# Kernel tuning notes

Measured on AMD Instinct MI355X. Metric: run time of the kernel, lower is better.

The kernel has to match this reference:

```python
import math
import jax, jax.numpy as jnp
import numpy as np

B, L, NS = 8, 1024, 512
D, NH, DN = 512, 8, 256
E, K, HE = 8, 2, 2048
EPS = 1e-5


def setup_inputs() -> dict:
    key = jax.random.key(0)
    ks = jax.random.split(key, 40)
    def rn(i, shape, s=0.02):
        return jax.random.normal(ks[i], shape, jnp.float32) * s
    inp = {
        'x': jax.random.normal(ks[0], (B, L, D), jnp.float32),
        'scene_tokens': jax.random.normal(ks[1], (B, NS, D), jnp.float32),
        't': jax.random.uniform(ks[2], (B,), jnp.float32) * 1000.0,
        # scene LayerNorm (affine)
        'scene_norm_g': jnp.ones((D,), jnp.float32),
        'scene_norm_b': jnp.zeros((D,), jnp.float32),
        # scene cross-attn projections (stored [in,out])
        'ca_wq': rn(3, (D, D)), 'ca_bq': jnp.zeros((D,)),
        'ca_wk': rn(4, (D, D)), 'ca_bk': jnp.zeros((D,)),
        'ca_wv': rn(5, (D, D)), 'ca_bv': jnp.zeros((D,)),
        'ca_wo': rn(6, (D, D)), 'ca_bo': jnp.zeros((D,)),
        # self-attn projections
        'sa_wq': rn(7, (D, D)), 'sa_bq': jnp.zeros((D,)),
        'sa_wk': rn(8, (D, D)), 'sa_bk': jnp.zeros((D,)),
        'sa_wv': rn(9, (D, D)), 'sa_bv': jnp.zeros((D,)),
        'sa_wo': rn(10, (D, D)), 'sa_bo': jnp.zeros((D,)),
        # noise_embed MLP: Linear(D,DN) -> SiLU -> Linear(DN,DN)
        'ne_w1': rn(11, (D, DN)), 'ne_b1': jnp.zeros((DN,)),
        'ne_w2': rn(12, (DN, DN)), 'ne_b2': jnp.zeros((DN,)),
        # AdaLN modulations: Linear(DN, 2D)
        'ncsa_mod_w': rn(13, (DN, 2 * D)), 'ncsa_mod_b': jnp.zeros((2 * D,)),
        'moe_mod_w': rn(14, (DN, 2 * D)), 'moe_mod_b': jnp.zeros((2 * D,)),
        # router
        'router_w': rn(15, (DN, E), s=0.1),
        # stacked pose-branch experts: fc_in D->2*HE, fc_out HE->D
        'fc_in_w': rn(16, (E, D, 2 * HE)), 'fc_in_b': jnp.zeros((E, 2 * HE)),
        'fc_out_w': rn(17, (E, HE, D)), 'fc_out_b': jnp.zeros((E, D)),
    }
    return inp


def _ln(x):
    mu = x.mean(-1, keepdims=True)
    var = ((x - mu) ** 2).mean(-1, keepdims=True)
    return (x - mu) * jax.lax.rsqrt(var + EPS)


def _mha(q_in, k_in, v_in, wq, bq, wk, bk, wv, bv, wo, bo):
    b, lq, d = q_in.shape
    lk = k_in.shape[1]
    hd = d // NH
    q = (q_in @ wq + bq).reshape(b, lq, NH, hd)
    k = (k_in @ wk + bk).reshape(b, lk, NH, hd)
    v = (v_in @ wv + bv).reshape(b, lk, NH, hd)
    att = jnp.einsum('bqhd,bkhd->bhqk', q, k) / math.sqrt(hd)
    p = jax.nn.softmax(att, axis=-1)
    o = jnp.einsum('bhqk,bkhd->bqhd', p, v).reshape(b, lq, d)
    return o @ wo + bo


def reference(x, scene_tokens, t,
              scene_norm_g, scene_norm_b,
              ca_wq, ca_bq, ca_wk, ca_bk, ca_wv, ca_bv, ca_wo, ca_bo,
              sa_wq, sa_bq, sa_wk, sa_bk, sa_wv, sa_bv, sa_wo, sa_bo,
              ne_w1, ne_b1, ne_w2, ne_b2,
              ncsa_mod_w, ncsa_mod_b, moe_mod_w, moe_mod_b,
              router_w, fc_in_w, fc_in_b, fc_out_w, fc_out_b):
    # --- noise clock embedding: sinusoidal(t, D) -> MLP ---
    half = D // 2
    freqs = jnp.exp(-math.log(10000.0) * jnp.arange(half, dtype=jnp.float32) / (half - 1))
    ang = t[:, None] * freqs[None, :]
    temb = jnp.concatenate([jnp.cos(ang), jnp.sin(ang)], axis=-1)  # [B, D]
    nc = jax.nn.silu(temb @ ne_w1 + ne_b1) @ ne_w2 + ne_b2  # [B, DN]

    # --- scene cross-attention ---
    x_in = _ln(x) * scene_norm_g + scene_norm_b
    x = x + _mha(x_in, scene_tokens, scene_tokens,
                 ca_wq, ca_bq, ca_wk, ca_bk, ca_wv, ca_bv, ca_wo, ca_bo)

    # --- noise-conditioned self-attention (AdaLN) ---
    mod = nc @ ncsa_mod_w + ncsa_mod_b
    shift, scale = jnp.split(mod, 2, axis=-1)
    x_ncsa = _ln(x) * (1.0 + scale[:, None, :]) + shift[:, None, :]
    x = x + _mha(x_ncsa, x_ncsa, x_ncsa,
                 sa_wq, sa_bq, sa_wk, sa_bk, sa_wv, sa_bv, sa_wo, sa_bo)

    # --- pose branch: AdaLN + noise-conditioned MoE ---
    mod = nc @ moe_mod_w + moe_mod_b
    shift, scale = jnp.split(mod, 2, axis=-1)
    x_moe = _ln(x) * (1.0 + scale[:, None, :]) + shift[:, None, :]

    logits = nc @ router_w  # temperature = 1.0
    probs = jax.nn.softmax(logits, axis=-1)
    tw, ti = jax.lax.top_k(probs, K)  # [B,K]
    tw = tw / jnp.clip(tw.sum(-1, keepdims=True), 1e-8)

    # gather per-sample selected expert weights -> grouped GEMM
    Wi = fc_in_w[ti]   # [B,K,D,2HE]
    bi = fc_in_b[ti]   # [B,K,2HE]
    h = jnp.einsum('bld,bkdh->bklh', x_moe, Wi) + bi[:, :, None, :]
    val, gate = jnp.split(h, 2, axis=-1)
    hid = val * jax.nn.silu(gate)   # [B,K,L,HE]
    Wo = fc_out_w[ti]  # [B,K,HE,D]
    bo = fc_out_b[ti]  # [B,K,D]
    eo = jnp.einsum('bklh,bkhd->bkld', hid, Wo) + bo[:, :, None, :]
    mixed = jnp.einsum('bk,bkld->bld', tw, eo)

    return x + mixed
```

## Files before the change

kernel.cpp:

```cpp
#include <hip/hip_runtime.h>
#include <math.h>

typedef unsigned short ushort_t;
typedef __attribute__((ext_vector_type(8))) short short8;
typedef __attribute__((ext_vector_type(4))) float f32x4;

#define B_   8
#define L_   1024
#define NS_  512
#define D_   512
#define NH_  8
#define HE_  2048
#define EPS_ 1e-5f

#define MFMA16(a, b, c) __builtin_amdgcn_mfma_f32_16x16x32_bf16(a, b, c, 0, 0, 0)
#define GL2LDS(g, l) __builtin_amdgcn_global_load_lds( \
    (const __attribute__((address_space(1))) unsigned int*)(g), \
    (__attribute__((address_space(3))) unsigned int*)(l), 16, 0, 0)

__device__ __forceinline__ ushort_t f2bf(float f) {
  unsigned u = __float_as_uint(f);
  unsigned r = (u + 0x7fffu + ((u >> 16) & 1u)) >> 16;
  return (ushort_t)r;
}

__device__ __forceinline__ void stage_tile(const ushort_t* __restrict__ g0,
                                           int ld, ushort_t* lds) {
  const int t = threadIdx.x;
  const int w = t >> 6, lane = t & 63;
#pragma unroll
  for (int j = 0; j < 2; ++j) {
    const int c = w * 64 + j * 256 + lane;
    const int row = c >> 2, col = (c & 3) * 8;
    GL2LDS(g0 + (size_t)row * ld + col, lds + (size_t)(w * 64 + j * 256) * 8);
  }
}

__device__ __forceinline__ void stage_tile64(const ushort_t* __restrict__ g0,
                                             int ld, ushort_t* lds) {
  const int t = threadIdx.x;
  const int w = t >> 6, lane = t & 63;
#pragma unroll
  for (int j = 0; j < 4; ++j) {
    const int c = w * 64 + j * 256 + lane;
    const int row = c >> 3;
    const int sc = (c & 7) ^ (row & 7);
    GL2LDS(g0 + (size_t)row * ld + sc * 8, lds + (size_t)(w * 64 + j * 256) * 8);
  }
}

__global__ __launch_bounds__(1024) void noise_embed(
    const float* __restrict__ t_in,
    const float* __restrict__ w1, const float* __restrict__ b1,
    const float* __restrict__ w2, const float* __restrict__ b2,
    const float* __restrict__ rw,
    float* __restrict__ nc_out,
    float* __restrict__ tw_out, int* __restrict__ ti_out)
{
  const int b = blockIdx.x;
  const int t = threadIdx.x;
  __shared__ float temb[512];
  __shared__ float h1[256];
  __shared__ float ncs[256];
  __shared__ float lg[8];
  const float tv = t_in[b];
  if (t < 512) {
    const int k = t & 255;
    float fr = __expf(-logf(10000.0f) * (float)k / 255.0f);
    float ang = tv * fr;
    temb[t] = (t < 256) ? cosf(ang) : sinf(ang);
  }
  __syncthreads();
  const int col = t >> 2, part = t & 3;
  {
    float s = 0.f;
    const float* wp = w1 + (size_t)(part * 128) * 256 + col;
    const float* tp = temb + part * 128;
#pragma unroll 32
    for (int i = 0; i < 128; ++i) s += tp[i] * wp[(size_t)i * 256];
    s += __shfl_xor(s, 1, 64);
    s += __shfl_xor(s, 2, 64);
    if (part == 0) {
      s += b1[col];
      h1[col] = s / (1.0f + __expf(-s));
    }
  }
  __syncthreads();
  {
    float s = 0.f;
    const float* wp = w2 + (size_t)(part * 64) * 256 + col;
    const float* hp = h1 + part * 64;
#pragma unroll 32
    for (int i = 0; i < 64; ++i) s += hp[i] * wp[(size_t)i * 256];
    s += __shfl_xor(s, 1, 64);
    s += __shfl_xor(s, 2, 64);
    if (part == 0) {
      s += b2[col];
      ncs[col] = s;
      nc_out[b * 256 + col] = s;
    }
  }
  __syncthreads();
  if (t < 64) {
    const int e = t >> 3, seg = t & 7;
    float s = 0.f;
#pragma unroll
    for (int i = 0; i < 32; ++i) s += ncs[seg * 32 + i] * rw[(seg * 32 + i) * 8 + e];
    s += __shfl_xor(s, 1, 64);
    s += __shfl_xor(s, 2, 64);
    s += __shfl_xor(s, 4, 64);
    if (seg == 0) lg[e] = s;
  }
  __syncthreads();
  if (t == 0) {
    float mx = lg[0];
    for (int e = 1; e < 8; ++e) mx = fmaxf(mx, lg[e]);
    float z = 0.f, p[8];
    for (int e = 0; e < 8; ++e) { p[e] = __expf(lg[e] - mx); z += p[e]; }
    for (int e = 0; e < 8; ++e) p[e] /= z;
    int i0 = 0;
    for (int e = 1; e < 8; ++e) if (p[e] > p[i0]) i0 = e;
    int i1 = (i0 == 0) ? 1 : 0;
    for (int e = 0; e < 8; ++e) if (e != i0 && p[e] > p[i1]) i1 = e;
    float s01 = fmaxf(p[i0] + p[i1], 1e-8f);
    tw_out[b * 2 + 0] = p[i0] / s01;
    tw_out[b * 2 + 1] = p[i1] / s01;
    ti_out[b * 2 + 0] = i0;
    ti_out[b * 2 + 1] = i1;
  }
}

__global__ __launch_bounds__(1024) void mod_proj(
    const float* __restrict__ nc,
    const float* __restrict__ ncsa_w, const float* __restrict__ ncsa_b,
    const float* __restrict__ moe_w, const float* __restrict__ moe_b,
    float* __restrict__ ncsa_mod, float* __restrict__ moe_mod)
{
  const int b = blockIdx.x, cg = blockIdx.y;
  const int t = threadIdx.x;
  __shared__ float ncs[256];
  if (t < 256) ncs[t] = nc[b * 256 + t];
  __syncthreads();
  const int idx = t >> 2, part = t & 3;
  const int half = idx >> 7;
  const int col = cg * 128 + (idx & 127);
  const float* wsel = half ? moe_w : ncsa_w;
  float s = 0.f;
  const float* wp = wsel + (size_t)(part * 64) * 1024 + col;
  const float* np = ncs + part * 64;
#pragma unroll 32
  for (int i = 0; i < 64; ++i) s += np[i] * wp[(size_t)i * 1024];
  s += __shfl_xor(s, 1, 64);
  s += __shfl_xor(s, 2, 64);
  if (part == 0) {
    const float* bsel = half ? moe_b : ncsa_b;
    float* osel = half ? moe_mod : ncsa_mod;
    osel[b * 1024 + col] = s + bsel[col];
  }
}

__global__ __launch_bounds__(256) void ln_mod_kernel(
    const float* __restrict__ X, const float* __restrict__ gvec,
    const float* __restrict__ bvec, const float* __restrict__ mod,
    ushort_t* __restrict__ Y)
{
  const int row = blockIdx.x;
  const int b = row >> 10;
  const int t = threadIdx.x;
  const float* xr = X + (size_t)row * 512;
  float2 v = *(const float2*)(xr + t * 2);
  float s = v.x + v.y;
  float q = v.x * v.x + v.y * v.y;
#pragma unroll
  for (int off = 32; off > 0; off >>= 1) {
    s += __shfl_down(s, off, 64);
    q += __shfl_down(q, off, 64);
  }
  __shared__ float ws_[4], wq_[4], smu[1], sinv[1];
  if ((t & 63) == 0) { ws_[t >> 6] = s; wq_[t >> 6] = q; }
  __syncthreads();
  if (t == 0) {
    float S = ws_[0] + ws_[1] + ws_[2] + ws_[3];
    float Q = wq_[0] + wq_[1] + wq_[2] + wq_[3];
    float mu = S * (1.0f / 512.0f);
    float var = Q * (1.0f / 512.0f) - mu * mu;
    smu[0] = mu;
    sinv[0] = rsqrtf(var + EPS_);
  }
  __syncthreads();
  const float mu = smu[0], inv = sinv[0];
  const int d0 = t * 2;
  float scx, scy, shx, shy;
  if (mod) {
    const float* mrow = mod + (size_t)b * 1024;
    scx = 1.0f + mrow[512 + d0]; scy = 1.0f + mrow[512 + d0 + 1];
    shx = mrow[d0];              shy = mrow[d0 + 1];
  } else {
    scx = gvec[d0]; scy = gvec[d0 + 1];
    shx = bvec[d0]; shy = bvec[d0 + 1];
  }
  float ox = (v.x - mu) * inv * scx + shx;
  float oy = (v.y - mu) * inv * scy + shy;
  unsigned pk = (unsigned)f2bf(ox) | ((unsigned)f2bf(oy) << 16);
  *(unsigned*)(Y + (size_t)row * 512 + d0) = pk;
}

__global__ __launch_bounds__(256) void transpose_cvt(
    const float* __restrict__ in, ushort_t* __restrict__ out,
    int R, int C, long ibs, long obs)
{
  __shared__ float tile[32][33];
  const float* src = in + (size_t)blockIdx.z * ibs;
  ushort_t* dst = out + (size_t)blockIdx.z * obs;
  const int c0 = blockIdx.x * 32, r0 = blockIdx.y * 32;
  const int tx = threadIdx.x & 31, ty = threadIdx.x >> 5;
  for (int rr = ty; rr < 32; rr += 8)
    tile[rr][tx] = src[(size_t)(r0 + rr) * C + c0 + tx];
  __syncthreads();
  for (int rr = ty; rr < 32; rr += 8)
    dst[(size_t)(c0 + rr) * R + r0 + tx] = f2bf(tile[tx][rr]);
}

struct P8 { const float* p[8]; };
__global__ __launch_bounds__(256) void transpose_cvt8(
    P8 srcs, ushort_t* __restrict__ out)
{
  __shared__ float tile[32][33];
  const float* src = srcs.p[blockIdx.z];
  ushort_t* dst = out + (size_t)blockIdx.z * 512 * 512;
  const int c0 = blockIdx.x * 32, r0 = blockIdx.y * 32;
  const int tx = threadIdx.x & 31, ty = threadIdx.x >> 5;
  for (int rr = ty; rr < 32; rr += 8)
    tile[rr][tx] = src[(size_t)(r0 + rr) * 512 + c0 + tx];
  __syncthreads();
  for (int rr = ty; rr < 32; rr += 8)
    dst[(size_t)(c0 + rr) * 512 + r0 + tx] = f2bf(tile[tx][rr]);
}

__global__ __launch_bounds__(256) void cvt_bf16(
    const float* __restrict__ in, ushort_t* __restrict__ out)
{
  const int i = (blockIdx.x * 256 + threadIdx.x) * 4;
  float4 v = *(const float4*)(in + i);
  uint2 pk;
  pk.x = (unsigned)f2bf(v.x) | ((unsigned)f2bf(v.y) << 16);
  pk.y = (unsigned)f2bf(v.z) | ((unsigned)f2bf(v.w) << 16);
  *(uint2*)(out + i) = pk;
}

struct B3 { const float* p[3]; };
__global__ __launch_bounds__(256) void gemm_bf16(
    const ushort_t* __restrict__ A, const ushort_t* __restrict__ Bt,
    B3 bias, const float* __restrict__ resid,
    void* __restrict__ Cout, int M, int N, int K, int bf16_out)
{
  __shared__ ushort_t As[2][8192];
  __shared__ ushort_t Bs[2][8192];
  const int t = threadIdx.x;
  const int w = t >> 6, lane = t & 63;
  const int quad = lane >> 4, r = lane & 15;
  const int sw = r & 7;
  const int wm = w >> 1, wn = w & 1;
  const int gx = gridDim.x;
  const int T = gx * gridDim.y;
  const int lid = blockIdx.x + gx * blockIdx.y;
  const int nl = (lid & 7) * (T >> 3) + (lid >> 3);
  const int bm = (nl / gx) * 128, bn = (nl % gx) * 128;
  f32x4 acc[4][4];
#pragma unroll
  for (int i = 0; i < 4; ++i)
#pragma unroll
    for (int j = 0; j < 4; ++j) acc[i][j] = (f32x4){0.f, 0.f, 0.f, 0.f};
  const ushort_t* Ab = A + (size_t)bm * K;
  const ushort_t* Bb = Bt + (size_t)bn * K;
  const int NIT = K >> 6;
  stage_tile64(Ab, K, As[0]);
  stage_tile64(Bb, K, Bs[0]);
  __syncthreads();
  for (int it = 0; it < NIT; ++it) {
    const int cur = it & 1;
    if (it + 1 < NIT) {
      stage_tile64(Ab + (it + 1) * 64, K, As[cur ^ 1]);
      stage_tile64(Bb + (it + 1) * 64, K, Bs[cur ^ 1]);
    }
#pragma unroll
    for (int ki = 0; ki < 2; ++ki) {
      const int ch = (((ki << 2) | quad) ^ sw) * 8;
      short8 af[4], bfg[4];
#pragma unroll
      for (int i = 0; i < 4; ++i)
        af[i] = *(const short8*)&As[cur][(wm * 64 + i * 16 + r) * 64 + ch];
#pragma unroll
      for (int j = 0; j < 4; ++j)
        bfg[j] = *(const short8*)&Bs[cur][(wn * 64 + j * 16 + r) * 64 + ch];
#pragma unroll
      for (int i = 0; i < 4; ++i)
#pragma unroll
        for (int j = 0; j < 4; ++j)
          acc[i][j] = MFMA16(af[i], bfg[j], acc[i][j]);
    }
    __syncthreads();
  }
  if (bf16_out) {
    ushort_t* Cb = (ushort_t*)Cout;
#pragma unroll
    for (int j = 0; j < 4; ++j) {
      const int col = bn + wn * 64 + j * 16 + r;
      const float bia = bias.p[col >> 9][col & 511];
#pragma unroll
      for (int i = 0; i < 4; ++i)
#pragma unroll
        for (int reg = 0; reg < 4; ++reg) {
          const int row = bm + wm * 64 + i * 16 + quad * 4 + reg;
          Cb[(size_t)row * N + col] = f2bf(acc[i][j][reg] + bia);
        }
    }
  } else {
    float* Cf = (float*)Cout;
#pragma unroll
    for (int j = 0; j < 4; ++j) {
      const int col = bn + wn * 64 + j * 16 + r;
      const float bia = bias.p[col >> 9][col & 511];
#pragma unroll
      for (int i = 0; i < 4; ++i)
#pragma unroll
        for (int reg = 0; reg < 4; ++reg) {
          const int row = bm + wm * 64 + i * 16 + quad * 4 + reg;
          float v = acc[i][j][reg] + bia;
          if (resid) v += resid[(size_t)row * N + col];
          Cf[(size_t)row * N + col] = v;
        }
    }
  }
}

__global__ __launch_bounds__(512, 4) void fattn_mfma(
    const ushort_t* __restrict__ Q, const ushort_t* __restrict__ Kmat,
    const ushort_t* __restrict__ V, ushort_t* __restrict__ O, int Lk,
    int ldq, int ldkv)
{
  __shared__ __align__(16) ushort_t Ks[64][72];
  __shared__ __align__(16) ushort_t Vt[64][72];
  __shared__ __align__(16) ushort_t Pt[8][16][72];
  const int t = threadIdx.x;
  const int w = t >> 6, lane = t & 63;
  const int quad = lane >> 4, r = lane & 15;
  const int bid = blockIdx.x;
  const int xcd = bid & 7, jj = bid >> 3;
  const int qi = jj & 7;
  const int g = xcd + 8 * (jj >> 3);
  const int h = g & 7, b = g >> 3;
  const int q0 = qi * 128;
  const size_t hoff = (size_t)h * 64;
  const ushort_t* Qb = Q + ((size_t)b * 1024 + q0) * ldq + hoff;
  const ushort_t* Kb = Kmat + (size_t)b * Lk * ldkv + hoff;
  const ushort_t* Vb = V + (size_t)b * Lk * ldkv + hoff;

  short8 qb[2];
#pragma unroll
  for (int ki = 0; ki < 2; ++ki)
    qb[ki] = *(const short8*)(Qb + (size_t)(w * 16 + r) * ldq +
                              ki * 32 + quad * 8);

  f32x4 oacc[4];
#pragma unroll
  for (int rt = 0; rt < 4; ++rt) oacc[rt] = (f32x4){0.f, 0.f, 0.f, 0.f};
  float m_ = -1e30f;
  float l_ = 0.f;

  uint4 kr, vr, kn, vn;
  const int dof = w * 8;
  auto ldkvf = [&](int k0, uint4& kp, uint4& vp) {
    kp = *(const uint4*)(Kb + (size_t)(k0 + lane) * ldkv + dof);
    vp = *(const uint4*)(Vb + (size_t)(k0 + lane) * ldkv + dof);
  };
  auto stkv = [&](const uint4& kp, const uint4& vp) {
    *(uint4*)&Ks[lane][dof] = kp;
    const ushort_t* vv = (const ushort_t*)&vp;
#pragma unroll
    for (int i = 0; i < 8; ++i) Vt[dof + i][lane] = vv[i];
  };

  ldkvf(0, kr, vr);
  const int nch = Lk >> 6;
  for (int c = 0; c < nch; ++c) {
    stkv(kr, vr);
    __syncthreads();
    if (c + 1 < nch) ldkvf((c + 1) << 6, kn, vn);

    f32x4 sacc[4];
#pragma unroll
    for (int rt = 0; rt < 4; ++rt) sacc[rt] = (f32x4){0.f, 0.f, 0.f, 0.f};
    __builtin_amdgcn_s_setprio(1);
#pragma unroll
    for (int ki = 0; ki < 2; ++ki) {
      short8 kf[4];
#pragma unroll
      for (int rt = 0; rt < 4; ++rt)
        kf[rt] = *(const short8*)&Ks[rt * 16 + r][ki * 32 + quad * 8];
#pragma unroll
      for (int rt = 0; rt < 4; ++rt)
        sacc[rt] = MFMA16(kf[rt], qb[ki], sacc[rt]);
    }
    __builtin_amdgcn_s_setprio(0);

    {
      float vmax = sacc[0][0];
#pragma unroll
      for (int rt = 0; rt < 4; ++rt)
#pragma unroll
        for (int reg = 0; reg < 4; ++reg) vmax = fmaxf(vmax, sacc[rt][reg]);
      vmax = fmaxf(vmax, __shfl_xor(vmax, 16, 64));
      vmax = fmaxf(vmax, __shfl_xor(vmax, 32, 64));
      const float pm = vmax * 0.125f;
      if (__any(pm > m_ + 8.f)) {
        const float mnew = fmaxf(m_, pm);
        const float corr = __expf(m_ - mnew);
        m_ = mnew;
        l_ *= corr;
#pragma unroll
        for (int rt = 0; rt < 4; ++rt)
#pragma unroll
          for (int reg = 0; reg < 4; ++reg) oacc[rt][reg] *= corr;
      }
      const float mcur = m_;
      float ps = 0.f;
#pragma unroll
      for (int rt = 0; rt < 4; ++rt) {
        float p0 = __expf(fmaf(sacc[rt][0], 0.125f, -mcur));
        float p1 = __expf(fmaf(sacc[rt][1], 0.125f, -mcur));
        float p2 = __expf(fmaf(sacc[rt][2], 0.125f, -mcur));
        float p3 = __expf(fmaf(sacc[rt][3], 0.125f, -mcur));
        ps += (p0 + p1) + (p2 + p3);
        uint2 pk;
        pk.x = (unsigned)f2bf(p0) | ((unsigned)f2bf(p1) << 16);
        pk.y = (unsigned)f2bf(p2) | ((unsigned)f2bf(p3) << 16);
        *(uint2*)&Pt[w][r][rt * 16 + quad * 4] = pk;
      }
      ps += __shfl_xor(ps, 16, 64);
      ps += __shfl_xor(ps, 32, 64);
      l_ += ps;
    }

    __builtin_amdgcn_s_setprio(1);
#pragma unroll
    for (int ki = 0; ki < 2; ++ki) {
      short8 vf[4], pf;
#pragma unroll
      for (int rt = 0; rt < 4; ++rt)
        vf[rt] = *(const short8*)&Vt[rt * 16 + r][ki * 32 + quad * 8];
      pf = *(const short8*)&Pt[w][r][ki * 32 + quad * 8];
#pragma unroll
      for (int rt = 0; rt < 4; ++rt)
        oacc[rt] = MFMA16(vf[rt], pf, oacc[rt]);
    }
    __builtin_amdgcn_s_setprio(0);
    __syncthreads();
    kr = kn; vr = vn;
  }

  {
    const float inv = 1.0f / l_;
    const int qg = q0 + w * 16 + r;
    ushort_t* op = O + ((size_t)b * 1024 + qg) * 512 + hoff;
#pragma unroll
    for (int rt = 0; rt < 4; ++rt) {
      uint2 pk;
      pk.x = (unsigned)f2bf(oacc[rt][0] * inv) |
             ((unsigned)f2bf(oacc[rt][1] * inv) << 16);
      pk.y = (unsigned)f2bf(oacc[rt][2] * inv) |
             ((unsigned)f2bf(oacc[rt][3] * inv) << 16);
      *(uint2*)(op + rt * 16 + quad * 4) = pk;
    }
  }
}

__global__ __launch_bounds__(256) void moe_fcin(
    const ushort_t* __restrict__ Xm, const ushort_t* __restrict__ WiT,
    const float* __restrict__ Bi, const float* __restrict__ tw,
    const int* __restrict__ ti, ushort_t* __restrict__ Hid, int ks)
{
  __shared__ ushort_t As[2][4096];
  __shared__ ushort_t Bv[2][4096];
  __shared__ ushort_t Bg[2][4096];
  const int t = threadIdx.x;
  const int w = t >> 6, lane = t & 63;
  const int quad = lane >> 4, r = lane & 15;
  const int wm = w >> 1, wn = w & 1;
  const int lid = blockIdx.x + 16 * blockIdx.y + 128 * blockIdx.z;
  const int nl = (lid & 7) * 128 + (lid >> 3);
  const int n0 = (nl & 15) * 128;
  const int r0 = ((nl >> 4) & 7) * 128;
  const int b = nl >> 7;
  const int e = ti[b * 2 + ks];
  const float wq = tw[b * 2 + ks];
  const ushort_t* Ab = Xm + ((size_t)b * 1024 + r0) * 512;
  const ushort_t* Wv = WiT + (size_t)e * 4096 * 512 + (size_t)n0 * 512;
  const ushort_t* Wg = Wv + (size_t)2048 * 512;
  f32x4 av[4][4], ag[4][4];
#pragma unroll
  for (int i = 0; i < 4; ++i)
#pragma unroll
    for (int j = 0; j < 4; ++j) {
      av[i][j] = (f32x4){0.f, 0.f, 0.f, 0.f};
      ag[i][j] = (f32x4){0.f, 0.f, 0.f, 0.f};
    }
  stage_tile(Ab, 512, As[0]);
  stage_tile(Wv, 512, Bv[0]);
  stage_tile(Wg, 512, Bg[0]);
  __syncthreads();
  for (int it = 0; it < 16; ++it) {
    const int cur = it & 1;
    if (it + 1 < 16) {
      stage_tile(Ab + (it + 1) * 32, 512, As[cur ^ 1]);
      stage_tile(Wv + (it + 1) * 32, 512, Bv[cur ^ 1]);
      stage_tile(Wg + (it + 1) * 32, 512, Bg[cur ^ 1]);
    }
    short8 af[4], bv[4], bg[4];
#pragma unroll
    for (int i = 0; i < 4; ++i)
      af[i] = *(const short8*)&As[cur][(wm * 64 + i * 16 + r) * 32 + quad * 8];
#pragma unroll
    for (int j = 0; j < 4; ++j) {
      bv[j] = *(const short8*)&Bv[cur][(wn * 64 + j * 16 + r) * 32 + quad * 8];
      bg[j] = *(const short8*)&Bg[cur][(wn * 64 + j * 16 + r) * 32 + quad * 8];
    }
#pragma unroll
    for (int i = 0; i < 4; ++i)
#pragma unroll
      for (int j = 0; j < 4; ++j) {
        av[i][j] = MFMA16(af[i], bv[j], av[i][j]);
        ag[i][j] = MFMA16(af[i], bg[j], ag[i][j]);
      }
    __syncthreads();
  }
  ushort_t* Hb = Hid + (size_t)b * 1024 * 2048;
#pragma unroll
  for (int j = 0; j < 4; ++j) {
    const int col = n0 + wn * 64 + j * 16 + r;
    const float bval = Bi[(size_t)e * 4096 + col];
    const float bgat = Bi[(size_t)e * 4096 + 2048 + col];
#pragma unroll
    for (int i = 0; i < 4; ++i)
#pragma unroll
      for (int reg = 0; reg < 4; ++reg) {
        const int lrow = r0 + wm * 64 + i * 16 + quad * 4 + reg;
        float vv = av[i][j][reg] + bval;
        float gg = ag[i][j][reg] + bgat;
        float hv = vv * (gg / (1.0f + __expf(-gg))) * wq;
        Hb[(size_t)lrow * 2048 + col] = f2bf(hv);
      }
  }
}

__global__ __launch_bounds__(256) void moe_fcout(
    const ushort_t* __restrict__ Hid, const ushort_t* __restrict__ WoT,
    const float* __restrict__ Bo, const float* __restrict__ X2,
    const float* __restrict__ tw, const int* __restrict__ ti,
    float* __restrict__ Out, int ks, int first)
{
  __shared__ ushort_t As[2][8192];
  __shared__ ushort_t Bs[2][8192];
  const int t = threadIdx.x;
  const int w = t >> 6, lane = t & 63;
  const int quad = lane >> 4, r = lane & 15;
  const int sw = r & 7;
  const int wm = w >> 1, wn = w & 1;
  const int lid = blockIdx.x;
  const int nl = (lid & 7) * 32 + (lid >> 3);
  const int n0 = (nl & 3) * 128;
  const int r0 = ((nl >> 2) & 7) * 128;
  const int b = nl >> 5;
  const int e = ti[b * 2 + ks];
  f32x4 acc[4][4];
#pragma unroll
  for (int i = 0; i < 4; ++i)
#pragma unroll
    for (int j = 0; j < 4; ++j) acc[i][j] = (f32x4){0.f, 0.f, 0.f, 0.f};
  const ushort_t* Ab = Hid + ((size_t)b * 1024 + r0) * 2048;
  const ushort_t* Bb = WoT + (size_t)e * 512 * 2048 + (size_t)n0 * 2048;
  stage_tile64(Ab, 2048, As[0]);
  stage_tile64(Bb, 2048, Bs[0]);
  __syncthreads();
  for (int it = 0; it < 32; ++it) {
    const int cur = it & 1;
    if (it + 1 < 32) {
      stage_tile64(Ab + (it + 1) * 64, 2048, As[cur ^ 1]);
      stage_tile64(Bb + (it + 1) * 64, 2048, Bs[cur ^ 1]);
    }
#pragma unroll
    for (int ki = 0; ki < 2; ++ki) {
      const int ch = (((ki << 2) | quad) ^ sw) * 8;
      short8 af[4], bfg[4];
#pragma unroll
      for (int i = 0; i < 4; ++i)
        af[i] = *(const short8*)&As[cur][(wm * 64 + i * 16 + r) * 64 + ch];
#pragma unroll
      for (int j = 0; j < 4; ++j)
        bfg[j] = *(const short8*)&Bs[cur][(wn * 64 + j * 16 + r) * 64 + ch];
#pragma unroll
      for (int i = 0; i < 4; ++i)
#pragma unroll
        for (int j = 0; j < 4; ++j)
          acc[i][j] = MFMA16(af[i], bfg[j], acc[i][j]);
    }
    __syncthreads();
  }
  const int e0 = ti[b * 2], e1 = ti[b * 2 + 1];
  const float tw0 = tw[b * 2], tw1 = tw[b * 2 + 1];
#pragma unroll
  for (int j = 0; j < 4; ++j) {
    const int col = n0 + wn * 64 + j * 16 + r;
    const float badd = first ? (tw0 * Bo[(size_t)e0 * 512 + col] +
                                tw1 * Bo[(size_t)e1 * 512 + col]) : 0.f;
#pragma unroll
    for (int i = 0; i < 4; ++i)
#pragma unroll
      for (int reg = 0; reg < 4; ++reg) {
        const size_t row = (size_t)b * 1024 + r0 + wm * 64 + i * 16 + quad * 4 + reg;
        const size_t idx = row * 512 + col;
        const float base = first ? X2[idx] : Out[idx];
        Out[idx] = base + acc[i][j][reg] + badd;
      }
  }
}

extern "C" void kernel_launch(void* const* d_in, const int* in_sizes, int n_in,
                              void* d_out, int out_size, void* d_ws, size_t ws_size,
                              hipStream_t stream) {
  const float* x        = (const float*)d_in[0];
  const float* scene    = (const float*)d_in[1];
  const float* t_in     = (const float*)d_in[2];
  const float* sn_g     = (const float*)d_in[3];
  const float* sn_b     = (const float*)d_in[4];
  const float* ca_wq    = (const float*)d_in[5];
  const float* ca_bq    = (const float*)d_in[6];
  const float* ca_wk    = (const float*)d_in[7];
  const float* ca_bk    = (const float*)d_in[8];
  const float* ca_wv    = (const float*)d_in[9];
  const float* ca_bv    = (const float*)d_in[10];
  const float* ca_wo    = (const float*)d_in[11];
  const float* ca_bo    = (const float*)d_in[12];
  const float* sa_wq    = (const float*)d_in[13];
  const float* sa_bq    = (const float*)d_in[14];
  const float* sa_wk    = (const float*)d_in[15];
  const float* sa_bk    = (const float*)d_in[16];
  const float* sa_wv    = (const float*)d_in[17];
  const float* sa_bv    = (const float*)d_in[18];
  const float* sa_wo    = (const float*)d_in[19];
  const float* sa_bo    = (const float*)d_in[20];
  const float* ne_w1    = (const float*)d_in[21];
  const float* ne_b1    = (const float*)d_in[22];
  const float* ne_w2    = (const float*)d_in[23];
  const float* ne_b2    = (const float*)d_in[24];
  const float* ncsa_w   = (const float*)d_in[25];
  const float* ncsa_b   = (const float*)d_in[26];
  const float* moe_w    = (const float*)d_in[27];
  const float* moe_b    = (const float*)d_in[28];
  const float* router_w = (const float*)d_in[29];
  const float* fc_in_w  = (const float*)d_in[30];
  const float* fc_in_b  = (const float*)d_in[31];
  const float* fc_out_w = (const float*)d_in[32];
  const float* fc_out_b = (const float*)d_in[33];
  float* out = (float*)d_out;

  char* W = (char*)d_ws;
  const size_t MB = 1u << 20;
  float* ncsa_mod = (float*)W;
  float* moe_mod  = ncsa_mod + 8192;
  float* tw       = moe_mod + 8192;
  int*   ti       = (int*)(tw + 16);
  float* nc_ws    = (float*)(ti + 16);
  ushort_t* wT      = (ushort_t*)(W + 1 * MB);
  ushort_t* fciT    = (ushort_t*)(W + 5 * MB);
  ushort_t* fcoT    = (ushort_t*)(W + 37 * MB);
  ushort_t* xin_bf  = (ushort_t*)(W + 53 * MB);
  ushort_t* attn_bf = xin_bf;
  ushort_t* scene_bf= (ushort_t*)(W + 61 * MB);
  ushort_t* cq  = (ushort_t*)(W + 65 * MB);
  ushort_t* ckv = (ushort_t*)(W + 73 * MB);
  ushort_t* qkv = (ushort_t*)(W + 65 * MB);
  ushort_t* hid = (ushort_t*)(W + 61 * MB);
  float* x1 = out;

  const int WSZ = 512 * 512;

  noise_embed<<<dim3(B_), dim3(1024), 0, stream>>>(
      t_in, ne_w1, ne_b1, ne_w2, ne_b2, router_w, nc_ws, tw, ti);
  mod_proj<<<dim3(B_, 8), dim3(1024), 0, stream>>>(
      nc_ws, ncsa_w, ncsa_b, moe_w, moe_b, ncsa_mod, moe_mod);

  P8 dsrc;
  dsrc.p[0] = ca_wq; dsrc.p[1] = ca_wk; dsrc.p[2] = ca_wv; dsrc.p[3] = ca_wo;
  dsrc.p[4] = sa_wq; dsrc.p[5] = sa_wk; dsrc.p[6] = sa_wv; dsrc.p[7] = sa_wo;
  transpose_cvt8<<<dim3(16, 16, 8), 256, 0, stream>>>(dsrc, wT);
  transpose_cvt<<<dim3(128, 16, 8), 256, 0, stream>>>(fc_in_w, fciT, 512, 4096,
                                                      (long)512 * 4096, (long)512 * 4096);
  transpose_cvt<<<dim3(16, 64, 8), 256, 0, stream>>>(fc_out_w, fcoT, 2048, 512,
                                                     (long)2048 * 512, (long)2048 * 512);
  cvt_bf16<<<dim3(2048), 256, 0, stream>>>(scene, scene_bf);

  B3 bq1 = {{ca_bq, ca_bq, ca_bq}};
  B3 bkv = {{ca_bk, ca_bv, ca_bv}};
  B3 bo3 = {{ca_bo, ca_bo, ca_bo}};
  ln_mod_kernel<<<dim3(8192), 256, 0, stream>>>(x, sn_g, sn_b, nullptr, xin_bf);
  gemm_bf16<<<dim3(4, 64), 256, 0, stream>>>(xin_bf, wT + 0 * WSZ, bq1, nullptr, cq, 8192, 512, 512, 1);
  gemm_bf16<<<dim3(8, 32), 256, 0, stream>>>(scene_bf, wT + 1 * WSZ, bkv, nullptr, ckv, 4096, 1024, 512, 1);
  fattn_mfma<<<dim3(512), dim3(512), 0, stream>>>(cq, ckv, ckv + 512, attn_bf, NS_, 512, 1024);
  gemm_bf16<<<dim3(4, 64), 256, 0, stream>>>(attn_bf, wT + 3 * WSZ, bo3, x, x1, 8192, 512, 512, 0);

  B3 bqkv = {{sa_bq, sa_bk, sa_bv}};
  B3 bso = {{sa_bo, sa_bo, sa_bo}};
  ln_mod_kernel<<<dim3(8192), 256, 0, stream>>>(x1, nullptr, nullptr, ncsa_mod, xin_bf);
  gemm_bf16<<<dim3(12, 64), 256, 0, stream>>>(xin_bf, wT + 4 * WSZ, bqkv, nullptr, qkv, 8192, 1536, 512, 1);
  fattn_mfma<<<dim3(512), dim3(512), 0, stream>>>(qkv, qkv + 512, qkv + 1024, attn_bf, L_, 1536, 1536);
  gemm_bf16<<<dim3(4, 64), 256, 0, stream>>>(attn_bf, wT + 7 * WSZ, bso, out, out, 8192, 512, 512, 0);

  ln_mod_kernel<<<dim3(8192), 256, 0, stream>>>(out, nullptr, nullptr, moe_mod, xin_bf);
  moe_fcin<<<dim3(16, 8, B_), 256, 0, stream>>>(xin_bf, fciT, fc_in_b, tw, ti, hid, 0);
  moe_fcout<<<dim3(256), 256, 0, stream>>>(hid, fcoT, fc_out_b, out, tw, ti, out, 0, 1);
  moe_fcin<<<dim3(16, 8, B_), 256, 0, stream>>>(xin_bf, fciT, fc_in_b, tw, ti, hid, 1);
  moe_fcout<<<dim3(256), 256, 0, stream>>>(hid, fcoT, fc_out_b, out, tw, ti, out, 1, 0);
}
```

Measured before the change: 678.7 us.

## Interleave MoE value/gate weight columns and use swizzled 64-wide K tiles in fc_in

The fc_in weight transpose now interleaves value and gate columns, so a single B tile covers both halves. Each lane pair exchanges value and gate through a lane shuffle in the epilogue to apply SiLU gating. The fc_in GEMM switches to 64-wide K staging with an XOR-swizzled LDS layout and a single accumulator set per block, with twice as many blocks. The aim is fewer LDS bank conflicts and fewer barriers per K step. In exchange, half the lanes sit idle during the epilogue stores and the stores become narrower.

```diff
diff --git a/kernel.cpp b/kernel.cpp
--- a/kernel.cpp
+++ b/kernel.cpp
@@ -221,6 +221,25 @@
     dst[(size_t)(c0 + rr) * R + r0 + tx] = f2bf(tile[tx][rr]);
 }
 
+__global__ __launch_bounds__(256) void transpose_cvt_ileave(
+    const float* __restrict__ in, ushort_t* __restrict__ out)
+{
+  __shared__ float tile[32][33];
+  const int e = blockIdx.z;
+  const int c0 = blockIdx.x * 32, d0 = blockIdx.y * 32;
+  const int tx = threadIdx.x & 31, ty = threadIdx.x >> 5;
+  const float* src = in + (size_t)e * 512 * 4096;
+  ushort_t* dst = out + (size_t)e * 4096 * 512;
+  const int sc = (c0 >> 1) + (tx & 15) + (tx >> 4) * 2048;
+  for (int rr = ty; rr < 32; rr += 8)
+    tile[rr][tx] = src[(size_t)(d0 + rr) * 4096 + sc];
+  __syncthreads();
+  for (int rr = ty; rr < 32; rr += 8) {
+    const int lsc = (rr >> 1) | ((rr & 1) << 4);
+    dst[(size_t)(c0 + rr) * 512 + d0 + tx] = f2bf(tile[tx][lsc]);
+  }
+}
+
 struct P8 { const float* p[8]; };
 __global__ __launch_bounds__(256) void transpose_cvt8(
     P8 srcs, ushort_t* __restrict__ out)
@@ -480,75 +499,72 @@
     const float* __restrict__ Bi, const float* __restrict__ tw,
     const int* __restrict__ ti, ushort_t* __restrict__ Hid, int ks)
 {
-  __shared__ ushort_t As[2][4096];
-  __shared__ ushort_t Bv[2][4096];
-  __shared__ ushort_t Bg[2][4096];
+  __shared__ ushort_t As[2][8192];
+  __shared__ ushort_t Bs[2][8192];
   const int t = threadIdx.x;
   const int w = t >> 6, lane = t & 63;
   const int quad = lane >> 4, r = lane & 15;
+  const int sw = r & 7;
   const int wm = w >> 1, wn = w & 1;
-  const int lid = blockIdx.x + 16 * blockIdx.y + 128 * blockIdx.z;
-  const int nl = (lid & 7) * 128 + (lid >> 3);
-  const int n0 = (nl & 15) * 128;
-  const int r0 = ((nl >> 4) & 7) * 128;
-  const int b = nl >> 7;
+  const int lid = blockIdx.x;
+  const int nl = (lid & 7) * 256 + (lid >> 3);
+  const int n0 = (nl & 31) * 128;
+  const int r0 = ((nl >> 5) & 7) * 128;
+  const int b = nl >> 8;
   const int e = ti[b * 2 + ks];
   const float wq = tw[b * 2 + ks];
+  f32x4 acc[4][4];
+#pragma unroll
+  for (int i = 0; i < 4; ++i)
+#pragma unroll
+    for (int j = 0; j < 4; ++j) acc[i][j] = (f32x4){0.f, 0.f, 0.f, 0.f};
   const ushort_t* Ab = Xm + ((size_t)b * 1024 + r0) * 512;
-  const ushort_t* Wv = WiT + (size_t)e * 4096 * 512 + (size_t)n0 * 512;
-  const ushort_t* Wg = Wv + (size_t)2048 * 512;
-  f32x4 av[4][4], ag[4][4];
-#pragma unroll
-  for (int i = 0; i < 4; ++i)
-#pragma unroll
-    for (int j = 0; j < 4; ++j) {
-      av[i][j] = (f32x4){0.f, 0.f, 0.f, 0.f};
-      ag[i][j] = (f32x4){0.f, 0.f, 0.f, 0.f};
-    }
-  stage_tile(Ab, 512, As[0]);
-  stage_tile(Wv, 512, Bv[0]);
-  stage_tile(Wg, 512, Bg[0]);
-  __syncthreads();
-  for (int it = 0; it < 16; ++it) {
+  const ushort_t* Bb = WiT + (size_t)e * 4096 * 512 + (size_t)n0 * 512;
+  stage_tile64(Ab, 512, As[0]);
+  stage_tile64(Bb, 512, Bs[0]);
+  __syncthreads();
+  for (int it = 0; it < 8; ++it) {
     const int cur = it & 1;
-    if (it + 1 < 16) {
-      stage_tile(Ab + (it + 1) * 32, 512, As[cur ^ 1]);
-      stage_tile(Wv + (it + 1) * 32, 512, Bv[cur ^ 1]);
-      stage_tile(Wg + (it + 1) * 32, 512, Bg[cur ^ 1]);
-    }
-    short8 af[4], bv[4], bg[4];
-#pragma unroll
-    for (int i = 0; i < 4; ++i)
-      af[i] = *(const short8*)&As[cur][(wm * 64 + i * 16 + r) * 32 + quad * 8];
-#pragma unroll
-    for (int j = 0; j < 4; ++j) {
-      bv[j] = *(const short8*)&Bv[cur][(wn * 64 + j * 16 + r) * 32 + quad * 8];
-      bg[j] = *(const short8*)&Bg[cur][(wn * 64 + j * 16 + r) * 32 + quad * 8];
-    }
-#pragma unroll
-    for (int i = 0; i < 4; ++i)
-#pragma unroll
-      for (int j = 0; j < 4; ++j) {
-        av[i][j] = MFMA16(af[i], bv[j], av[i][j]);
-        ag[i][j] = MFMA16(af[i], bg[j], ag[i][j]);
-      }
+    if (it + 1 < 8) {
+      stage_tile64(Ab + (it + 1) * 64, 512, As[cur ^ 1]);
+      stage_tile64(Bb + (it + 1) * 64, 512, Bs[cur ^ 1]);
+    }
+#pragma unroll
+    for (int ki = 0; ki < 2; ++ki) {
+      const int ch = (((ki << 2) | quad) ^ sw) * 8;
+      short8 af[4], bfg[4];
+#pragma unroll
+      for (int i = 0; i < 4; ++i)
+        af[i] = *(const short8*)&As[cur][(wm * 64 + i * 16 + r) * 64 + ch];
+#pragma unroll
+      for (int j = 0; j < 4; ++j)
+        bfg[j] = *(const short8*)&Bs[cur][(wn * 64 + j * 16 + r) * 64 + ch];
+#pragma unroll
+      for (int i = 0; i < 4; ++i)
+#pragma unroll
+        for (int j = 0; j < 4; ++j)
+          acc[i][j] = MFMA16(af[i], bfg[j], acc[i][j]);
+    }
     __syncthreads();
   }
   ushort_t* Hb = Hid + (size_t)b * 1024 * 2048;
 #pragma unroll
   for (int j = 0; j < 4; ++j) {
     const int col = n0 + wn * 64 + j * 16 + r;
-    const float bval = Bi[(size_t)e * 4096 + col];
-    const float bgat = Bi[(size_t)e * 4096 + 2048 + col];
+    const int oc = col >> 1;
+    const float bia = Bi[(size_t)e * 4096 + oc + (col & 1) * 2048];
 #pragma unroll
     for (int i = 0; i < 4; ++i)
 #pragma unroll
       for (int reg = 0; reg < 4; ++reg) {
-        const int lrow = r0 + wm * 64 + i * 16 + quad * 4 + reg;
-        float vv = av[i][j][reg] + bval;
-        float gg = ag[i][j][reg] + bgat;
-        float hv = vv * (gg / (1.0f + __expf(-gg))) * wq;
-        Hb[(size_t)lrow * 2048 + col] = f2bf(hv);
+        const float mine = acc[i][j][reg] + bia;
+        const float part = __shfl_xor(mine, 1, 64);
+        if ((r & 1) == 0) {
+          const float gg = part;
+          const float hv = mine * (gg / (1.0f + __expf(-gg))) * wq;
+          const int lrow = r0 + wm * 64 + i * 16 + quad * 4 + reg;
+          Hb[(size_t)lrow * 2048 + oc] = f2bf(hv);
+        }
       }
   }
 }
@@ -694,8 +710,7 @@
   dsrc.p[0] = ca_wq; dsrc.p[1] = ca_wk; dsrc.p[2] = ca_wv; dsrc.p[3] = ca_wo;
   dsrc.p[4] = sa_wq; dsrc.p[5] = sa_wk; dsrc.p[6] = sa_wv; dsrc.p[7] = sa_wo;
   transpose_cvt8<<<dim3(16, 16, 8), 256, 0, stream>>>(dsrc, wT);
-  transpose_cvt<<<dim3(128, 16, 8), 256, 0, stream>>>(fc_in_w, fciT, 512, 4096,
-                                                      (long)512 * 4096, (long)512 * 4096);
+  transpose_cvt_ileave<<<dim3(128, 16, 8), 256, 0, stream>>>(fc_in_w, fciT);
   transpose_cvt<<<dim3(16, 64, 8), 256, 0, stream>>>(fc_out_w, fcoT, 2048, 512,
                                                      (long)2048 * 512, (long)2048 * 512);
   cvt_bf16<<<dim3(2048), 256, 0, stream>>>(scene, scene_bf);
@@ -717,8 +732,8 @@
   gemm_bf16<<<dim3(4, 64), 256, 0, stream>>>(attn_bf, wT + 7 * WSZ, bso, out, out, 8192, 512, 512, 0);
 
   ln_mod_kernel<<<dim3(8192), 256, 0, stream>>>(out, nullptr, nullptr, moe_mod, xin_bf);
-  moe_fcin<<<dim3(16, 8, B_), 256, 0, stream>>>(xin_bf, fciT, fc_in_b, tw, ti, hid, 0);
+  moe_fcin<<<dim3(2048), 256, 0, stream>>>(xin_bf, fciT, fc_in_b, tw, ti, hid, 0);
   moe_fcout<<<dim3(256), 256, 0, stream>>>(hid, fcoT, fc_out_b, out, tw, ti, out, 0, 1);
-  moe_fcin<<<dim3(16, 8, B_), 256, 0, stream>>>(xin_bf, fciT, fc_in_b, tw, ti, hid, 1);
+  moe_fcin<<<dim3(2048), 256, 0, stream>>>(xin_bf, fciT, fc_in_b, tw, ti, hid, 1);
   moe_fcout<<<dim3(256), 256, 0, stream>>>(hid, fcoT, fc_out_b, out, tw, ti, out, 1, 0);
 }
```

After: 700.4 us. +3.2%, slower.
